# Optimization experiments

Measured on AMD Instinct MI355X. Metric: run time of the kernel, lower is better.

The kernel has to match this reference:

```python
import jax, jax.numpy as jnp
import numpy as np

# ---- dimensions ----
N_MOL, N_PER = 256, 32
N = N_MOL * N_PER                      # 8192 nodes
E = N_MOL * N_PER * (N_PER - 1)        # 253952 fully-connected directed edges
SDIM, VDIM, EDIM = 256, 64, 32
NAF, NBT, LAT = 16, 5, 64
LAYERS = 5
MSG_IN = 2 * SDIM + EDIM + 2           # [s_i, s_j, e, d, a]
MSG_OUT = SDIM + VDIM + 1 + EDIM       # scalar msg, vec weights, pos weight, edge update
BOND_IN = SDIM + EDIM + 1
BOND_HID = 128


def _block_fc_edges():
    # fully-connected (no self loops) edges within each molecule of N_PER atoms
    idx = np.arange(N_PER)
    src, tgt = np.meshgrid(idx, idx, indexing='ij')
    mask = src != tgt
    src, tgt = src[mask], tgt[mask]
    offs = (np.arange(N_MOL) * N_PER)[:, None]
    S = (src[None, :] + offs).reshape(-1)
    T = (tgt[None, :] + offs).reshape(-1)
    return np.stack([S, T], 0).astype(np.int64)


def setup_inputs() -> dict:
    key = jax.random.key(0)
    ks = jax.random.split(key, 16)
    edge_index = jnp.asarray(_block_fc_edges())
    batch = jnp.asarray(np.repeat(np.arange(N_MOL), N_PER).astype(np.int64))
    return dict(
        x=jax.random.normal(ks[0], (N, NAF), jnp.float32),
        z=jax.random.normal(ks[1], (N, LAT), jnp.float32),
        rot=jax.random.normal(ks[2], (N_MOL, 3, 3), jnp.float32),
        edge_index_global=edge_index,
        edge_attr_global=jax.random.normal(ks[3], (E, NBT), jnp.float32),
        batch=batch,
        # atom/bond input mappings (DenseLayer == Linear)
        Wam=jax.random.normal(ks[4], (NAF + LAT, SDIM + 3), jnp.float32) * 0.05,
        bam=jnp.zeros((SDIM + 3,), jnp.float32),
        Wbm=jax.random.normal(ks[5], (NBT, EDIM), jnp.float32) * 0.3,
        bbm=jnp.zeros((EDIM,), jnp.float32),
        # stacked per-layer EQGAT message-MLP weights
        gW1=jax.random.normal(ks[6], (LAYERS, MSG_IN, SDIM), jnp.float32) * 0.03,
        gb1=jnp.zeros((LAYERS, SDIM), jnp.float32),
        gW2=jax.random.normal(ks[7], (LAYERS, SDIM, MSG_OUT), jnp.float32) * 0.05,
        gb2=jnp.zeros((LAYERS, MSG_OUT), jnp.float32),
        # prediction heads
        Wh1=jax.random.normal(ks[8], (SDIM, SDIM), jnp.float32) * 0.05,
        bh1=jnp.zeros((SDIM,), jnp.float32),
        Wh2=jax.random.normal(ks[9], (SDIM, NAF), jnp.float32) * 0.05,
        bh2=jnp.zeros((NAF,), jnp.float32),
        We1=jax.random.normal(ks[10], (BOND_IN, BOND_HID), jnp.float32) * 0.05,
        be1=jnp.zeros((BOND_HID,), jnp.float32),
        We2=jax.random.normal(ks[11], (BOND_HID, NBT), jnp.float32) * 0.05,
        be2=jnp.zeros((NBT,), jnp.float32),
    )


def _edge_attrs(pos, src, tgt):
    # faithful to Decoder.calculate_edge_attrs (sqrt=True)
    r = pos[tgt] - pos[src]                       # [E,3]
    a = jnp.sum(pos[tgt] * pos[src], -1)          # [E]
    d = jnp.sqrt(jnp.clip(jnp.sum(r * r, -1), 1e-6))
    r_norm = r / (1.0 + d)[:, None]
    return d, a, r_norm


def reference(x, z, rot, edge_index_global, edge_attr_global, batch,
              Wam, bam, Wbm, bbm, gW1, gb1, gW2, gb2,
              Wh1, bh1, Wh2, bh2, We1, be1, We2, be2):
    src, tgt = edge_index_global[0], edge_index_global[1]
    n = x.shape[0]
    # atom mapping + split into scalar feats and positions
    h = jnp.concatenate([x, z], -1) @ Wam + bam
    s, pos = h[:, :SDIM], h[:, SDIM:]
    # per-graph rotation of positions
    pos = jnp.einsum('bij,bj->bi', rot[batch], pos)
    # bond mapping
    e = edge_attr_global @ Wbm + bbm
    v = jnp.zeros((n, 3, VDIM), x.dtype)
    # segment-mean denominator (in-degree), fixed since edge_index is fixed
    cnt = jnp.clip(jax.ops.segment_sum(jnp.ones((src.shape[0],), x.dtype), tgt,
                                       num_segments=n), 1.0)

    def seg_mean(m):
        out = jax.ops.segment_sum(m, tgt, num_segments=n)
        return out / cnt.reshape((n,) + (1,) * (m.ndim - 1))

    def layer(carry, p):
        s, v, pos, e = carry
        W1, b1, W2, b2 = p
        d, a, r_norm = _edge_attrs(pos, src, tgt)   # recompute_edge_attributes=True
        feat = jnp.concatenate([s[src], s[tgt], e, d[:, None], a[:, None]], -1)
        hdn = jax.nn.silu(feat @ W1 + b1)
        m = hdn @ W2 + b2
        m_s = m[:, :SDIM]
        m_v = m[:, SDIM:SDIM + VDIM]
        m_p = m[:, SDIM + VDIM:SDIM + VDIM + 1]
        m_e = m[:, SDIM + VDIM + 1:]
        s = s + seg_mean(m_s)                                   # scalar update
        v = v + seg_mean(r_norm[:, :, None] * m_v[:, None, :])  # equivariant vec update
        pos = pos + seg_mean(r_norm * m_p)                      # equivariant pos update
        e = e + m_e                                             # edge feature update
        return (s, v, pos, e), None

    (s, v, pos, e), _ = jax.lax.scan(layer, (s, v, pos, e), (gW1, gb1, gW2, gb2))

    # prediction head: atom logits, bond logits (symmetric s_i+s_j), coords
    atoms = jax.nn.silu(s @ Wh1 + bh1) @ Wh2 + bh2
    d, a, r_norm = _edge_attrs(pos, src, tgt)
    ef = jnp.concatenate([s[src] + s[tgt], e, d[:, None]], -1)
    bonds = jax.nn.silu(ef @ We1 + be1) @ We2 + be2
    return atoms, bonds, pos
```

## Files before the change

### kernel.cpp

```cpp
#include <hip/hip_runtime.h>
#include <hip/hip_bf16.h>
#include <cstdint>
#include <cstddef>

#define N_MOLS 256
#define NN     8192
#define SDIM_  256
#define NAF_   16
#define LAYERS_ 5

typedef __attribute__((ext_vector_type(8)))  short bf16x8;
typedef __attribute__((ext_vector_type(16))) float f32x16;
typedef __attribute__((ext_vector_type(4)))  float f32x4;

__device__ __forceinline__ float silu_f(float x) {
    return x * __builtin_amdgcn_rcpf(1.f + __expf(-x));
}
__device__ __forceinline__ short bfc(float f) {
    __hip_bfloat16 h = __float2bfloat16(f);
    return __builtin_bit_cast(short, h);
}
__device__ __forceinline__ float bf2f(short h) {
    union { uint32_t u; float f; } v; v.u = ((uint32_t)(unsigned short)h) << 16; return v.f;
}
#define ONEBF ((short)0x3F80)

#define OFF_T1    0
#define OFF_W2ST  655360
#define OFF_WH1T  983040
#define OFF_WE1T  1048576
#define OFF_W1CG  1081344
#define OFF_W1DA  1122304
#define OFF_W2P   1124864
#define OFF_W2EI  1126144
#define OFF_WE1CG 1167104
#define OFF_WD    1171200
#define OFF_WE2I  1171328
#define W_TOTAL   1175424

__global__ __launch_bounds__(256) void prep_weights(
    const float* __restrict__ gW1, const float* __restrict__ gW2,
    const float* __restrict__ Wh1, const float* __restrict__ We1,
    const float* __restrict__ We2, short* __restrict__ wb)
{
    for (int o = blockIdx.x * 256 + threadIdx.x; o < W_TOTAL; o += gridDim.x * 256) {
        float v;
        if (o < OFF_W2ST) {
            const int l = o >> 17, r = o & 131071;
            const int j2 = r >> 8, k = r & 255;
            v = gW1[(size_t)l * 139776 + (size_t)((j2 >> 8) * 256 + k) * 256 + (j2 & 255)];
        } else if (o < OFF_WH1T) {
            const int q = o - OFF_W2ST;
            const int l = q >> 16, r = q & 65535;
            const int n = r >> 8, k = r & 255;
            v = gW2[(size_t)l * 90368 + (size_t)k * 353 + n];
        } else if (o < OFF_WE1T) {
            const int q = o - OFF_WH1T;
            v = Wh1[(size_t)(q & 255) * 256 + (q >> 8)];
        } else if (o < OFF_W1CG) {
            const int q = o - OFF_WE1T;
            v = We1[(size_t)(q & 255) * 128 + (q >> 8)];
        } else if (o < OFF_W1DA) {
            const int q = o - OFF_W1CG;
            const int l = q >> 13, r = q & 8191;
            const int j = r >> 5, w = r & 31;
            v = gW1[(size_t)l * 139776 + (size_t)(512 + w) * 256 + j];
        } else if (o < OFF_W2P) {
            const int q = o - OFF_W1DA;
            const int l = q >> 9, r = q & 511;
            v = gW1[(size_t)l * 139776 + (size_t)(544 + (r >> 8)) * 256 + (r & 255)];
        } else if (o < OFF_W2EI) {
            const int q = o - OFF_W2P;
            v = gW2[(size_t)(q >> 8) * 90368 + (size_t)(q & 255) * 353 + 320];
        } else if (o < OFF_WE1CG) {
            const int q = o - OFF_W2EI;
            const int l = q >> 13, r = q & 8191;
            const int kk = r >> 9, lanei = (r >> 3) & 63, jj = r & 7;
            const int j = kk * 16 + (lanei >> 5) * 8 + jj;
            v = gW2[(size_t)l * 90368 + (size_t)j * 353 + 321 + (lanei & 31)];
        } else if (o < OFF_WD) {
            const int q = o - OFF_WE1CG;
            v = We1[(size_t)(256 + (q & 31)) * 128 + (q >> 5)];
        } else if (o < OFF_WE2I) {
            v = We1[288 * 128 + (o - OFF_WD)];
        } else {
            const int q = o - OFF_WE2I;
            const int kk = q >> 9, lanei = (q >> 3) & 63, jj = q & 7;
            const int c = lanei & 31;
            v = (c < 5) ? We2[(size_t)(kk * 16 + (lanei >> 5) * 8 + jj) * 5 + c] : 0.f;
        }
        wb[o] = bfc(v);
    }
}

__global__ __launch_bounds__(256) void node_init2(
    const float* __restrict__ x, const float* __restrict__ z,
    const float* __restrict__ rot, const float* __restrict__ Wam,
    const float* __restrict__ bam, float* __restrict__ s,
    short* __restrict__ sbf, float* __restrict__ pos)
{
    const int mol = blockIdx.x, t = threadIdx.x;
    __shared__ __align__(16) float xz[32][80];
    __shared__ float praw[32][3];
    for (int idx = t; idx < 32 * 80; idx += 256) {
        const int i = idx / 80, k = idx % 80;
        xz[i][k] = (k < 16) ? x[(size_t)(mol * 32 + i) * 16 + k]
                            : z[(size_t)(mol * 32 + i) * 64 + (k - 16)];
    }
    __syncthreads();
    float acc[32];
    #pragma unroll
    for (int i = 0; i < 32; ++i) acc[i] = 0.f;
    for (int k0 = 0; k0 < 80; k0 += 4) {
        const float w0 = Wam[(k0 + 0) * 259 + t];
        const float w1 = Wam[(k0 + 1) * 259 + t];
        const float w2 = Wam[(k0 + 2) * 259 + t];
        const float w3 = Wam[(k0 + 3) * 259 + t];
        #pragma unroll
        for (int i = 0; i < 32; ++i) {
            const float4 xv = *(const float4*)&xz[i][k0];
            acc[i] += xv.x * w0 + xv.y * w1 + xv.z * w2 + xv.w * w3;
        }
    }
    const float bv = bam[t];
    #pragma unroll
    for (int i = 0; i < 32; ++i) {
        const float v = acc[i] + bv;
        s[(size_t)(mol * 32 + i) * 256 + t] = v;
        sbf[(size_t)(mol * 32 + i) * 256 + t] = bfc(v);
    }
    if (t < 96) {
        const int i = t / 3, c = t % 3;
        float a2 = bam[256 + c];
        for (int k = 0; k < 80; ++k) a2 += xz[i][k] * Wam[k * 259 + 256 + c];
        praw[i][c] = a2;
    }
    __syncthreads();
    if (t < 96) {
        const int i = t / 3, c = t % 3;
        float p = 0.f;
        for (int jj = 0; jj < 3; ++jj) p += rot[mol * 9 + c * 3 + jj] * praw[i][jj];
        pos[(size_t)(mol * 32 + i) * 3 + c] = p;
    }
}

__global__ __launch_bounds__(256) void edge_init3(
    const float* __restrict__ ea, const float* __restrict__ Wbm,
    const float* __restrict__ bbm, short* __restrict__ ebuf)
{
    const int mol = blockIdx.x, t = threadIdx.x;
    __shared__ float sEa[4960];
    __shared__ float sW[5][32];
    __shared__ float sB[32];
    const float* base = ea + (size_t)mol * 4960;
    for (int i = t; i < 4960; i += 256) sEa[i] = base[i];
    if (t < 160) sW[t / 32][t & 31] = Wbm[t];
    if (t < 32)  sB[t] = bbm[t];
    __syncthreads();
    for (int i = t; i < 31744; i += 256) {
        const int c = i & 31;
        const int rrn = i >> 5;
        const int n = rrn / 31, rr = rrn - n * 31;
        const int s_ = rr + (rr >= n ? 1 : 0);
        const int gl = s_ * 31 + (n - (n > s_ ? 1 : 0));
        float acc = sB[c];
        #pragma unroll
        for (int k = 0; k < 5; ++k) acc += sEa[gl * 5 + k] * sW[k][c];
        ebuf[(size_t)mol * 31744 + i] = bfc(acc);
    }
}

template<int ACT, int OUTBF>
__global__ __launch_bounds__(256) void gemm_mfma(
    const short* __restrict__ A, const short* __restrict__ BT,
    void* __restrict__ Cv, const float* __restrict__ bias,
    int K, int N, float alpha)
{
    const int n0 = blockIdx.x * 64, m0 = blockIdx.y * 128;
    const int t = threadIdx.x;
    const int wave = t >> 6, lane = t & 63;
    const int l = lane & 31, half = lane >> 5;
    const int wm = wave & 1, wn = wave >> 1;
    __shared__ __align__(16) short sA[128][40];
    __shared__ __align__(16) short sBt[64][40];
    f32x16 acc0 = {}, acc1 = {};
    const int mA = t >> 1, koA = (t & 1) * 16;
    const int nB = t & 63, kqB = (t >> 6) * 8;
    for (int k0 = 0; k0 < K; k0 += 32) {
        {
            const short* ap = A + (size_t)(m0 + mA) * K + k0 + koA;
            *(bf16x8*)&sA[mA][koA]     = *(const bf16x8*)(ap);
            *(bf16x8*)&sA[mA][koA + 8] = *(const bf16x8*)(ap + 8);
        }
        {
            const short* bp = BT + (size_t)(n0 + nB) * K + k0 + kqB;
            *(bf16x8*)&sBt[nB][kqB] = *(const bf16x8*)bp;
        }
        __syncthreads();
        #pragma unroll
        for (int ks = 0; ks < 2; ++ks) {
            const bf16x8 bfrag = *(const bf16x8*)&sBt[wn * 32 + l][ks * 16 + half * 8];
            const bf16x8 afr0  = *(const bf16x8*)&sA[wm * 64 + l][ks * 16 + half * 8];
            const bf16x8 afr1  = *(const bf16x8*)&sA[wm * 64 + 32 + l][ks * 16 + half * 8];
            acc0 = __builtin_amdgcn_mfma_f32_32x32x16_bf16(afr0, bfrag, acc0, 0,0,0);
            acc1 = __builtin_amdgcn_mfma_f32_32x32x16_bf16(afr1, bfrag, acc1, 0,0,0);
        }
        __syncthreads();
    }
    const int n = n0 + wn * 32 + l;
    const float bv = bias ? bias[n] : 0.f;
    #pragma unroll
    for (int r = 0; r < 16; ++r) {
        const int row = (r & 3) + 8 * (r >> 2) + 4 * half;
        #pragma unroll
        for (int h = 0; h < 2; ++h) {
            const int m = m0 + wm * 64 + h * 32 + row;
            float v = alpha * (h ? acc1[r] : acc0[r]) + bv;
            if (ACT) v = silu_f(v);
            if (OUTBF) ((short*)Cv)[(size_t)m * N + n] = bfc(v);
            else       ((float*)Cv)[(size_t)m * N + n] = v;
        }
    }
}

__global__ __launch_bounds__(512) void edge_mfma(
    const short* __restrict__ sbfA, const short* __restrict__ T1,
    const float* __restrict__ posIn, float* __restrict__ posOut,
    short* __restrict__ ebuf,
    const short* __restrict__ W1cG, const short* __restrict__ W1daP,
    const short* __restrict__ W2pP, const short* __restrict__ W2eimg,
    const short* __restrict__ W2sT,
    const float* __restrict__ b1, const float* __restrict__ b2,
    float* __restrict__ s, short* __restrict__ sbfOut)
{
    const int blk = blockIdx.x;
    const int mol = blk >> 1;
    const int nbase = (blk & 1) * 16;
    const int t = threadIdx.x;
    const int wave = t >> 6, lane = t & 63;
    const int l = lane & 31, half = lane >> 5;
    const int node0 = mol * 32;

    __shared__ __align__(16) short sBg[256][72];
    __shared__ __align__(16) short sM[8][32][40];
    __shared__ __align__(16) short sHrows[16][264];
    __shared__ __align__(16) short sSB[16][264];
    __shared__ float sPosS[32][4];
    __shared__ __align__(16) short sW1da[2][256];
    __shared__ __align__(16) short sW2p[256];
    __shared__ float sP[8][32];
    __shared__ float sPd[16][4];
    short* sSbf = &sM[0][0][0];

    {
        const int j = t & 255, gh = t >> 8;
        const bf16x8 v0 = *(const bf16x8*)&W1cG[j * 32 + gh * 16];
        const bf16x8 v1 = *(const bf16x8*)&W1cG[j * 32 + gh * 16 + 8];
        const int c3 = (j >> 3) & 3;
        const int s0 = ((gh * 2 + 0) + 3 * c3) & 7;
        const int s1 = ((gh * 2 + 1) + 3 * c3) & 7;
        *(bf16x8*)&sBg[j][s0 * 8] = v0;
        *(bf16x8*)&sBg[j][s1 * 8] = v1;
    }
    {
        const int row = t >> 4, ch = (t & 15) * 16;
        const short* src = sbfA + (size_t)(node0 + row) * 256 + ch;
        *(bf16x8*)&sSbf[row * 264 + ch]     = *(const bf16x8*)(src);
        *(bf16x8*)&sSbf[row * 264 + ch + 8] = *(const bf16x8*)(src + 8);
    }
    if (t < 64) {
        short* d = &sW1da[0][0];
        *(bf16x8*)&d[t * 8] = *(const bf16x8*)&W1daP[t * 8];
    }
    if (t < 32) *(bf16x8*)&sW2p[t * 8] = *(const bf16x8*)&W2pP[t * 8];
    if (t < 96) sPosS[t / 3][t % 3] = posIn[node0 * 3 + t];
    __syncthreads();

    {
        const int jt = wave;
        const int j = jt * 32 + l;
        f32x16 accA = {}, accB = {};
        #pragma unroll
        for (int k0 = 0; k0 < 256; k0 += 16) {
            const bf16x8 afr = *(const bf16x8*)&sSbf[l * 264 + k0 + half * 8];
            const bf16x8 bA  = *(const bf16x8*)(T1 + (size_t)(j) * 256 + k0 + half * 8);
            const bf16x8 bB  = *(const bf16x8*)(T1 + (size_t)(256 + j) * 256 + k0 + half * 8);
            accA = __builtin_amdgcn_mfma_f32_32x32x16_bf16(afr, bA, accA, 0,0,0);
            accB = __builtin_amdgcn_mfma_f32_32x32x16_bf16(afr, bB, accB, 0,0,0);
        }
        const int c3 = (j >> 3) & 3;
        #pragma unroll
        for (int r = 0; r < 16; ++r) {
            const int node = (r & 3) + 8 * (r >> 2) + 4 * half;
            const int k = 32 + node;
            const int slot = ((k >> 3) + 3 * c3) & 7;
            sBg[j][slot * 8 + (k & 7)] = bfc(accA[r]);
            const int nl = node - nbase;
            if ((unsigned)nl < 16u) sSB[nl][j] = bfc(accB[r]);
        }
    }
    __syncthreads();

    bf16x8 w2efr[16];
    #pragma unroll
    for (int kk = 0; kk < 16; ++kk)
        w2efr[kk] = *(const bf16x8*)&W2eimg[(size_t)(kk * 64 + lane) * 8];
    float b1v[8];
    short w1dv[8], w1av[8];
    #pragma unroll
    for (int cb = 0; cb < 8; ++cb) {
        b1v[cb]  = b1[cb * 32 + l];
        w1dv[cb] = sW1da[0][cb * 32 + l];
        w1av[cb] = sW1da[1][cb * 32 + l];
    }
    const float b2e = b2[321 + l];
    const float b2p = b2[320];
    int bslot[4];
    #pragma unroll
    for (int ks = 0; ks < 4; ++ks)
        bslot[ks] = ((ks * 2 + half) + 3 * ((l >> 3) & 3)) & 7;

    for (int ni = 0; ni < 2; ++ni) {
        const int n = nbase + wave + ni * 8;
        const int nloc = wave + ni * 8;
        const int rrc = (l < 31) ? l : 30;
        const int src = rrc + (rrc >= n ? 1 : 0);
        const float ax = sPosS[n][0],  ay = sPosS[n][1],  az = sPosS[n][2];
        const float bx = sPosS[src][0], by = sPosS[src][1], bz = sPosS[src][2];
        const float rx = ax - bx, ry = ay - by, rz = az - bz;
        const float av = ax * bx + ay * by + az * bz;
        const float dd = sqrtf(fmaxf(rx * rx + ry * ry + rz * rz, 1e-6f));
        const float inv = __builtin_amdgcn_rcpf(1.f + dd);
        const float rnx = rx * inv, rny = ry * inv, rnz = rz * inv;

        const short* ebase = ebuf + ((size_t)((mol * 32 + n) * 31 + l)) * 32;
        const bf16x8 fr0 = *(const bf16x8*)(ebase + half * 8);
        const bf16x8 fr1 = *(const bf16x8*)(ebase + 16 + half * 8);
        bf16x8 fr2 = {}, fr3, fr4;
        if (half == 0) { fr2[0] = bfc(dd); fr2[1] = bfc(av); }
        #pragma unroll
        for (int jj = 0; jj < 8; ++jj) {
            fr3[jj] = (half * 8 + jj == src)      ? ONEBF : (short)0;
            fr4[jj] = (16 + half * 8 + jj == src) ? ONEBF : (short)0;
        }

        f32x16 accC = {}, accP = {};
        float Hacc[8];

        const int g = l >> 3, jlow = l & 7;
        #pragma unroll
        for (int cb = 0; cb < 8; ++cb) {
            const float sbv = bf2f(sSB[nloc][cb * 32 + l]) + b1v[cb];
            f32x16 acc;
            #pragma unroll
            for (int r = 0; r < 16; ++r) acc[r] = sbv;
            {
                const short* brow = &sBg[cb * 32 + l][0];
                __builtin_amdgcn_s_setprio(1);
                acc = __builtin_amdgcn_mfma_f32_32x32x16_bf16(fr0, *(const bf16x8*)(brow + bslot[0]*8), acc, 0,0,0);
                acc = __builtin_amdgcn_mfma_f32_32x32x16_bf16(fr1, *(const bf16x8*)(brow + bslot[1]*8), acc, 0,0,0);
                acc = __builtin_amdgcn_mfma_f32_32x32x16_bf16(fr3, *(const bf16x8*)(brow + bslot[2]*8), acc, 0,0,0);
                acc = __builtin_amdgcn_mfma_f32_32x32x16_bf16(fr4, *(const bf16x8*)(brow + bslot[3]*8), acc, 0,0,0);
                bf16x8 frB2 = {};
                if (half == 0) { frB2[0] = w1dv[cb]; frB2[1] = w1av[cb]; }
                acc = __builtin_amdgcn_mfma_f32_32x32x16_bf16(fr2, frB2, acc, 0,0,0);
                __builtin_amdgcn_s_setprio(0);
            }
            float hs = 0.f;
            #pragma unroll
            for (int r = 0; r < 16; ++r) {
                const int e = (r & 3) + 8 * (r >> 2) + 4 * half;
                float h = silu_f(acc[r]);
                if (half == 1 && r == 15) h = 0.f;
                hs += h;
                sM[wave][e][((g + (e >> 3)) & 3) * 8 + jlow] = bfc(h);
            }
            Hacc[cb] = hs;
            #pragma unroll
            for (int q = 0; q < 2; ++q) {
                const bf16x8 afr  = *(const bf16x8*)&sM[wave][l][((q * 2 + half + (l >> 3)) & 3) * 8];
                const bf16x8 wpfr = *(const bf16x8*)&sW2p[cb * 32 + q * 16 + half * 8];
                accC = __builtin_amdgcn_mfma_f32_32x32x16_bf16(afr, w2efr[cb * 2 + q], accC, 0,0,0);
                accP = __builtin_amdgcn_mfma_f32_32x32x16_bf16(afr, wpfr, accP, 0,0,0);
            }
        }
        #pragma unroll
        for (int cb = 0; cb < 8; ++cb) {
            const float v = Hacc[cb] + __shfl_xor(Hacc[cb], 32, 64);
            if (lane < 32) sHrows[nloc][cb * 32 + lane] = bfc(v);
        }
        if (l == 0) {
            #pragma unroll
            for (int q4 = 0; q4 < 4; ++q4) {
                float4 pv = { accP[q4 * 4 + 0], accP[q4 * 4 + 1],
                              accP[q4 * 4 + 2], accP[q4 * 4 + 3] };
                *(float4*)&sP[wave][q4 * 8 + 4 * half] = pv;
            }
        }
        const float pown = sP[wave][l];
        const float pfull = (half == 0 && l < 31) ? (pown + b2p) : 0.f;
        float pd0 = rnx * pfull, pd1 = rny * pfull, pd2 = rnz * pfull;
        #pragma unroll
        for (int m = 1; m <= 32; m <<= 1) {
            pd0 += __shfl_xor(pd0, m, 64);
            pd1 += __shfl_xor(pd1, m, 64);
            pd2 += __shfl_xor(pd2, m, 64);
        }
        if (lane == 0) {
            sPd[nloc][0] = pd0;
            sPd[nloc][1] = pd1;
            sPd[nloc][2] = pd2;
        }
        #pragma unroll
        for (int r = 0; r < 16; ++r) {
            const int e = (r & 3) + 8 * (r >> 2) + 4 * half;
            if (e < 31) {
                short* ep = ebuf + ((size_t)((mol * 32 + n) * 31 + e)) * 32 + l;
                *ep = bfc(bf2f(*ep) + accC[r] + b2e);
            }
        }
    }

    __syncthreads();

    {
        const int jb0 = wave * 32;
        const int arow = lane & 15, kg = lane >> 4;
        f32x4 accS0 = {}, accS1 = {};
        #pragma unroll
        for (int k0 = 0; k0 < 256; k0 += 32) {
            const bf16x8 afr = *(const bf16x8*)&sHrows[arow][k0 + kg * 8];
            const bf16x8 bf0 = *(const bf16x8*)&W2sT[(size_t)(jb0 + arow) * 256 + k0 + kg * 8];
            const bf16x8 bf1 = *(const bf16x8*)&W2sT[(size_t)(jb0 + 16 + arow) * 256 + k0 + kg * 8];
            accS0 = __builtin_amdgcn_mfma_f32_16x16x32_bf16(afr, bf0, accS0, 0,0,0);
            accS1 = __builtin_amdgcn_mfma_f32_16x16x32_bf16(afr, bf1, accS1, 0,0,0);
        }
        const int col = lane & 15;
        const int orow = (lane >> 4) * 4;
        const float bv0 = b2[jb0 + col];
        const float bv1 = b2[jb0 + 16 + col];
        #pragma unroll
        for (int r = 0; r < 4; ++r) {
            const int node = node0 + nbase + orow + r;
            {
                float* sp = s + (size_t)node * 256 + jb0 + col;
                const float nv = *sp + accS0[r] * (1.f / 31.f) + bv0;
                *sp = nv;
                sbfOut[(size_t)node * 256 + jb0 + col] = bfc(nv);
            }
            {
                float* sp = s + (size_t)node * 256 + jb0 + 16 + col;
                const float nv = *sp + accS1[r] * (1.f / 31.f) + bv1;
                *sp = nv;
                sbfOut[(size_t)node * 256 + jb0 + 16 + col] = bfc(nv);
            }
        }
    }
    if (t < 48) {
        const int nl = t / 3, c = t % 3;
        const int node = node0 + nbase + nl;
        posOut[(size_t)node * 3 + c] = posIn[(size_t)node * 3 + c] + sPd[nl][c] * (1.f / 31.f);
    }
}

__global__ __launch_bounds__(512) void bond_mfma(
    const short* __restrict__ sbfA, const short* __restrict__ We1T,
    const float* __restrict__ pos, short* __restrict__ ebuf,
    const short* __restrict__ We1cG, const short* __restrict__ WdP,
    const short* __restrict__ We2img,
    const float* __restrict__ be1, const float* __restrict__ be2,
    float* __restrict__ outB, float* __restrict__ outPos)
{
    const int blk = blockIdx.x;
    const int mol = blk >> 1;
    const int nbase = (blk & 1) * 16;
    const int t = threadIdx.x;
    const int wave = t >> 6, lane = t & 63;
    const int l = lane & 31, half = lane >> 5;
    const int node0 = mol * 32;

    __shared__ __align__(16) short sBg2[128][72];
    __shared__ __align__(16) short sHdnB[8][32][40];
    __shared__ __align__(16) short sU[32][136];
    __shared__ float sPosS[32][4];
    __shared__ __align__(16) short sWd[128];
    short* sSbf = &sHdnB[0][0][0];

    {
        const int j = t & 127, g = t >> 7;
        const bf16x8 v = *(const bf16x8*)&We1cG[j * 32 + g * 8];
        const int slot = (g + 3 * ((j >> 3) & 3)) & 7;
        *(bf16x8*)&sBg2[j][slot * 8] = v;
    }
    {
        const int row = t >> 4, ch = (t & 15) * 16;
        const short* src = sbfA + (size_t)(node0 + row) * 256 + ch;
        *(bf16x8*)&sSbf[row * 264 + ch]     = *(const bf16x8*)(src);
        *(bf16x8*)&sSbf[row * 264 + ch + 8] = *(const bf16x8*)(src + 8);
    }
    if (t < 16) *(bf16x8*)&sWd[t * 8] = *(const bf16x8*)&WdP[t * 8];
    if (t < 96) sPosS[t / 3][t % 3] = pos[node0 * 3 + t];
    __syncthreads();

    if (wave < 4) {
        const int j = wave * 32 + l;
        f32x16 accU = {};
        #pragma unroll
        for (int k0 = 0; k0 < 256; k0 += 16) {
            const bf16x8 afr = *(const bf16x8*)&sSbf[l * 264 + k0 + half * 8];
            const bf16x8 bU  = *(const bf16x8*)(We1T + (size_t)j * 256 + k0 + half * 8);
            accU = __builtin_amdgcn_mfma_f32_32x32x16_bf16(afr, bU, accU, 0,0,0);
        }
        const int c3 = (j >> 3) & 3;
        #pragma unroll
        for (int r = 0; r < 16; ++r) {
            const int node = (r & 3) + 8 * (r >> 2) + 4 * half;
            const short uv = bfc(accU[r]);
            const int k = 32 + node;
            const int slot = ((k >> 3) + 3 * c3) & 7;
            sBg2[j][slot * 8 + (k & 7)] = uv;
            sU[node][j] = uv;
        }
    }

    bf16x8 w2fr[8];
    #pragma unroll
    for (int kk = 0; kk < 8; ++kk)
        w2fr[kk] = *(const bf16x8*)&We2img[(size_t)(kk * 64 + lane) * 8];
    float be1v[4];
    #pragma unroll
    for (int cb = 0; cb < 4; ++cb) be1v[cb] = be1[cb * 32 + l];
    const float be2v = (l < 5) ? be2[l] : 0.f;
    int bslot[4];
    #pragma unroll
    for (int ks = 0; ks < 4; ++ks)
        bslot[ks] = ((ks * 2 + half) + 3 * ((l >> 3) & 3)) & 7;
    __syncthreads();

    for (int ni = 0; ni < 2; ++ni) {
        const int n = nbase + wave + ni * 8;
        const int rrc = (l < 31) ? l : 30;
        const int src = rrc + (rrc >= n ? 1 : 0);
        const float rx = sPosS[n][0] - sPosS[src][0];
        const float ry = sPosS[n][1] - sPosS[src][1];
        const float rz = sPosS[n][2] - sPosS[src][2];
        const float dd = sqrtf(fmaxf(rx * rx + ry * ry + rz * rz, 1e-6f));

        const short* ebase = ebuf + ((size_t)((mol * 32 + n) * 31 + l)) * 32;
        const bf16x8 fr0 = *(const bf16x8*)(ebase + half * 8);
        const bf16x8 fr1 = *(const bf16x8*)(ebase + 16 + half * 8);
        bf16x8 fr2 = {}, fr3, fr4;
        if (half == 0) fr2[0] = bfc(dd);
        #pragma unroll
        for (int jj = 0; jj < 8; ++jj) {
            fr3[jj] = (half * 8 + jj == src)      ? ONEBF : (short)0;
            fr4[jj] = (16 + half * 8 + jj == src) ? ONEBF : (short)0;
        }

        f32x16 accC = {};
        const int g = l >> 3, jlow = l & 7;
        #pragma unroll
        for (int cb = 0; cb < 4; ++cb) {
            const float uin = bf2f(sU[n][cb * 32 + l]) + be1v[cb];
            f32x16 acc;
            #pragma unroll
            for (int r = 0; r < 16; ++r) acc[r] = uin;
            {
                const short* brow = &sBg2[cb * 32 + l][0];
                acc = __builtin_amdgcn_mfma_f32_32x32x16_bf16(fr0, *(const bf16x8*)(brow + bslot[0]*8), acc, 0,0,0);
                acc = __builtin_amdgcn_mfma_f32_32x32x16_bf16(fr1, *(const bf16x8*)(brow + bslot[1]*8), acc, 0,0,0);
                acc = __builtin_amdgcn_mfma_f32_32x32x16_bf16(fr3, *(const bf16x8*)(brow + bslot[2]*8), acc, 0,0,0);
                acc = __builtin_amdgcn_mfma_f32_32x32x16_bf16(fr4, *(const bf16x8*)(brow + bslot[3]*8), acc, 0,0,0);
                bf16x8 frWd = {};
                if (half == 0) frWd[0] = sWd[cb * 32 + l];
                acc = __builtin_amdgcn_mfma_f32_32x32x16_bf16(fr2, frWd, acc, 0,0,0);
            }
            #pragma unroll
            for (int r = 0; r < 16; ++r) {
                const int e = (r & 3) + 8 * (r >> 2) + 4 * half;
                sHdnB[wave][e][((g + (e >> 3)) & 3) * 8 + jlow] = bfc(silu_f(acc[r]));
            }
            #pragma unroll
            for (int q = 0; q < 2; ++q) {
                const bf16x8 afr = *(const bf16x8*)&sHdnB[wave][l][((q * 2 + half + (l >> 3)) & 3) * 8];
                accC = __builtin_amdgcn_mfma_f32_32x32x16_bf16(afr, w2fr[cb * 2 + q], accC, 0,0,0);
            }
        }
        if (l < 5) {
            #pragma unroll
            for (int r = 0; r < 16; ++r) {
                const int e = (r & 3) + 8 * (r >> 2) + 4 * half;
                if (e < 31) {
                    const int s_ = e + (e >= n ? 1 : 0);
                    const int ge = (mol * 32 + s_) * 31 + (n - (n > s_ ? 1 : 0));
                    outB[(size_t)ge * 5 + l] = accC[r] + be2v;
                }
            }
        }
    }
    if (t < 48) {
        const int nl = t / 3, c = t % 3;
        const int node = node0 + nbase + nl;
        outPos[(size_t)node * 3 + c] = pos[(size_t)node * 3 + c];
    }
}

__global__ __launch_bounds__(256) void atoms_kernel(
    const short* __restrict__ tmp, const float* __restrict__ Wh2,
    const float* __restrict__ bh2, float* __restrict__ outA)
{
    const int t = threadIdx.x;
    __shared__ __align__(16) float sW[256][17];
    for (int i = t; i < 256 * 4; i += 256) {
        const int k = i >> 2, c4 = (i & 3) * 4;
        const float4 w = *(const float4*)&Wh2[k * 16 + c4];
        sW[k][c4 + 0] = w.x; sW[k][c4 + 1] = w.y;
        sW[k][c4 + 2] = w.z; sW[k][c4 + 3] = w.w;
    }
    __syncthreads();
    const int gid = blockIdx.x * 256 + t;
    const int n = gid >> 4, o = gid & 15;
    float acc = bh2[o];
    for (int k0 = 0; k0 < 256; k0 += 8) {
        const bf16x8 a = *(const bf16x8*)&tmp[(size_t)n * 256 + k0];
        #pragma unroll
        for (int j = 0; j < 8; ++j)
            acc += bf2f(a[j]) * sW[k0 + j][o];
    }
    outA[gid] = acc;
}

extern "C" void kernel_launch(void* const* d_in, const int* in_sizes, int n_in,
                              void* d_out, int out_size, void* d_ws, size_t ws_size,
                              hipStream_t stream) {
    const float* x   = (const float*)d_in[0];
    const float* z   = (const float*)d_in[1];
    const float* rot = (const float*)d_in[2];
    const float* ea  = (const float*)d_in[4];
    const float* Wam = (const float*)d_in[6];
    const float* bam = (const float*)d_in[7];
    const float* Wbm = (const float*)d_in[8];
    const float* bbm = (const float*)d_in[9];
    const float* gW1 = (const float*)d_in[10];
    const float* gb1 = (const float*)d_in[11];
    const float* gW2 = (const float*)d_in[12];
    const float* gb2 = (const float*)d_in[13];
    const float* Wh1 = (const float*)d_in[14];
    const float* bh1 = (const float*)d_in[15];
    const float* Wh2 = (const float*)d_in[16];
    const float* bh2 = (const float*)d_in[17];
    const float* We1 = (const float*)d_in[18];
    const float* be1 = (const float*)d_in[19];
    const float* We2 = (const float*)d_in[20];
    const float* be2 = (const float*)d_in[21];
    float* out = (float*)d_out;

    float* ws  = (float*)d_ws;
    float* s    = ws;
    float* pos  = ws + 2097152;
    short* e    = (short*)(ws + 2121728);
    short* wb   = (short*)(ws + 6184960);
    short* sbf0 = (short*)(ws + 6772672);
    short* sbf1 = (short*)(ws + 10248192);
    short* tmph = (short*)(ws + 12345344);
    float* pos2 = ws + 16539648;

    prep_weights<<<1024, 256, 0, stream>>>(gW1, gW2, Wh1, We1, We2, wb);
    node_init2<<<N_MOLS, 256, 0, stream>>>(x, z, rot, Wam, bam, s, sbf0, pos);
    edge_init3<<<N_MOLS, 256, 0, stream>>>(ea, Wbm, bbm, e);

    float* pbuf[2] = { pos, pos2 };
    short* sbb[2] = { sbf0, sbf1 };
    for (int l = 0; l < LAYERS_; ++l) {
        const float* b1 = gb1 + l * 256;
        const float* b2 = gb2 + l * 353;
        edge_mfma<<<2 * N_MOLS, 512, 0, stream>>>(
            sbb[l & 1], wb + OFF_T1 + (size_t)l * 131072,
            pbuf[l & 1], pbuf[(l + 1) & 1], e,
            wb + OFF_W1CG + l * 8192, wb + OFF_W1DA + l * 512,
            wb + OFF_W2P + l * 256, wb + OFF_W2EI + l * 8192,
            wb + OFF_W2ST + (size_t)l * 65536,
            b1, b2, s, sbb[(l + 1) & 1]);
    }
    float* posF = pbuf[LAYERS_ & 1];
    short* sbfF = sbb[LAYERS_ & 1];

    gemm_mfma<1,1><<<dim3(4, 64), 256, 0, stream>>>(
        sbfF, wb + OFF_WH1T, tmph, bh1, 256, 256, 1.f);
    atoms_kernel<<<512, 256, 0, stream>>>(tmph, Wh2, bh2, out);

    bond_mfma<<<2 * N_MOLS, 512, 0, stream>>>(
        sbfF, wb + OFF_WE1T, posF, e, wb + OFF_WE1CG, wb + OFF_WD,
        wb + OFF_WE2I, be1, be2, out + 131072, out + 131072 + 1269760);
}
```

Before: 669.0 us.

## Merge init kernels into one launch and fold atom head into bond kernel

The three setup kernels (weight prep, node init, edge init) become a single launch that picks its role from the block index. The atom prediction head (a 256x256 silu layer followed by a 256x16 layer) moves from a separate GEMM and atoms kernel into the tail of the bond kernel, computed with 16x16 MFMAs on the block's node tile. A bf16 copy of Wh2 is added to the packed weight buffer for this. The aim is to cut kernel launches and the global round trip of the hidden activation, at the cost of a longer bond-kernel epilogue that reuses its shared buffers.

```diff
diff --git a/kernel.cpp b/kernel.cpp
--- a/kernel.cpp
+++ b/kernel.cpp
@@ -36,189 +36,138 @@
 #define OFF_WE1CG 1167104
 #define OFF_WD    1171200
 #define OFF_WE2I  1171328
-#define W_TOTAL   1175424
-
-__global__ __launch_bounds__(256) void prep_weights(
+#define OFF_WH2T  1175424
+#define W_TOTAL   1179520
+
+__global__ __launch_bounds__(256) void init_all(
+    const float* __restrict__ x, const float* __restrict__ z,
+    const float* __restrict__ rot, const float* __restrict__ Wam,
+    const float* __restrict__ bam, const float* __restrict__ ea,
+    const float* __restrict__ Wbm, const float* __restrict__ bbm,
     const float* __restrict__ gW1, const float* __restrict__ gW2,
     const float* __restrict__ Wh1, const float* __restrict__ We1,
-    const float* __restrict__ We2, short* __restrict__ wb)
+    const float* __restrict__ We2, const float* __restrict__ Wh2,
+    float* __restrict__ s, short* __restrict__ sbf, float* __restrict__ pos,
+    short* __restrict__ ebuf, short* __restrict__ wb)
 {
-    for (int o = blockIdx.x * 256 + threadIdx.x; o < W_TOTAL; o += gridDim.x * 256) {
-        float v;
-        if (o < OFF_W2ST) {
-            const int l = o >> 17, r = o & 131071;
-            const int j2 = r >> 8, k = r & 255;
-            v = gW1[(size_t)l * 139776 + (size_t)((j2 >> 8) * 256 + k) * 256 + (j2 & 255)];
-        } else if (o < OFF_WH1T) {
-            const int q = o - OFF_W2ST;
-            const int l = q >> 16, r = q & 65535;
-            const int n = r >> 8, k = r & 255;
-            v = gW2[(size_t)l * 90368 + (size_t)k * 353 + n];
-        } else if (o < OFF_WE1T) {
-            const int q = o - OFF_WH1T;
-            v = Wh1[(size_t)(q & 255) * 256 + (q >> 8)];
-        } else if (o < OFF_W1CG) {
-            const int q = o - OFF_WE1T;
-            v = We1[(size_t)(q & 255) * 128 + (q >> 8)];
-        } else if (o < OFF_W1DA) {
-            const int q = o - OFF_W1CG;
-            const int l = q >> 13, r = q & 8191;
-            const int j = r >> 5, w = r & 31;
-            v = gW1[(size_t)l * 139776 + (size_t)(512 + w) * 256 + j];
-        } else if (o < OFF_W2P) {
-            const int q = o - OFF_W1DA;
-            const int l = q >> 9, r = q & 511;
-            v = gW1[(size_t)l * 139776 + (size_t)(544 + (r >> 8)) * 256 + (r & 255)];
-        } else if (o < OFF_W2EI) {
-            const int q = o - OFF_W2P;
-            v = gW2[(size_t)(q >> 8) * 90368 + (size_t)(q & 255) * 353 + 320];
-        } else if (o < OFF_WE1CG) {
-            const int q = o - OFF_W2EI;
-            const int l = q >> 13, r = q & 8191;
-            const int kk = r >> 9, lanei = (r >> 3) & 63, jj = r & 7;
-            const int j = kk * 16 + (lanei >> 5) * 8 + jj;
-            v = gW2[(size_t)l * 90368 + (size_t)j * 353 + 321 + (lanei & 31)];
-        } else if (o < OFF_WD) {
-            const int q = o - OFF_WE1CG;
-            v = We1[(size_t)(256 + (q & 31)) * 128 + (q >> 5)];
-        } else if (o < OFF_WE2I) {
-            v = We1[288 * 128 + (o - OFF_WD)];
-        } else {
-            const int q = o - OFF_WE2I;
-            const int kk = q >> 9, lanei = (q >> 3) & 63, jj = q & 7;
-            const int c = lanei & 31;
-            v = (c < 5) ? We2[(size_t)(kk * 16 + (lanei >> 5) * 8 + jj) * 5 + c] : 0.f;
-        }
-        wb[o] = bfc(v);
-    }
-}
-
-__global__ __launch_bounds__(256) void node_init2(
-    const float* __restrict__ x, const float* __restrict__ z,
-    const float* __restrict__ rot, const float* __restrict__ Wam,
-    const float* __restrict__ bam, float* __restrict__ s,
-    short* __restrict__ sbf, float* __restrict__ pos)
-{
-    const int mol = blockIdx.x, t = threadIdx.x;
-    __shared__ __align__(16) float xz[32][80];
-    __shared__ float praw[32][3];
-    for (int idx = t; idx < 32 * 80; idx += 256) {
-        const int i = idx / 80, k = idx % 80;
-        xz[i][k] = (k < 16) ? x[(size_t)(mol * 32 + i) * 16 + k]
-                            : z[(size_t)(mol * 32 + i) * 64 + (k - 16)];
-    }
-    __syncthreads();
-    float acc[32];
-    #pragma unroll
-    for (int i = 0; i < 32; ++i) acc[i] = 0.f;
-    for (int k0 = 0; k0 < 80; k0 += 4) {
-        const float w0 = Wam[(k0 + 0) * 259 + t];
-        const float w1 = Wam[(k0 + 1) * 259 + t];
-        const float w2 = Wam[(k0 + 2) * 259 + t];
-        const float w3 = Wam[(k0 + 3) * 259 + t];
+    __shared__ __align__(16) char smem[20608];
+    const int b = blockIdx.x, t = threadIdx.x;
+    if (b < 1024) {
+        for (int o = b * 256 + t; o < W_TOTAL; o += 1024 * 256) {
+            float v;
+            if (o < OFF_W2ST) {
+                const int l = o >> 17, r = o & 131071;
+                const int j2 = r >> 8, k = r & 255;
+                v = gW1[(size_t)l * 139776 + (size_t)((j2 >> 8) * 256 + k) * 256 + (j2 & 255)];
+            } else if (o < OFF_WH1T) {
+                const int q = o - OFF_W2ST;
+                const int l = q >> 16, r = q & 65535;
+                const int n = r >> 8, k = r & 255;
+                v = gW2[(size_t)l * 90368 + (size_t)k * 353 + n];
+            } else if (o < OFF_WE1T) {
+                const int q = o - OFF_WH1T;
+                v = Wh1[(size_t)(q & 255) * 256 + (q >> 8)];
+            } else if (o < OFF_W1CG) {
+                const int q = o - OFF_WE1T;
+                v = We1[(size_t)(q & 255) * 128 + (q >> 8)];
+            } else if (o < OFF_W1DA) {
+                const int q = o - OFF_W1CG;
+                const int l = q >> 13, r = q & 8191;
+                const int j = r >> 5, w = r & 31;
+                v = gW1[(size_t)l * 139776 + (size_t)(512 + w) * 256 + j];
+            } else if (o < OFF_W2P) {
+                const int q = o - OFF_W1DA;
+                const int l = q >> 9, r = q & 511;
+                v = gW1[(size_t)l * 139776 + (size_t)(544 + (r >> 8)) * 256 + (r & 255)];
+            } else if (o < OFF_W2EI) {
+                const int q = o - OFF_W2P;
+                v = gW2[(size_t)(q >> 8) * 90368 + (size_t)(q & 255) * 353 + 320];
+            } else if (o < OFF_WE1CG) {
+                const int q = o - OFF_W2EI;
+                const int l = q >> 13, r = q & 8191;
+                const int kk = r >> 9, lanei = (r >> 3) & 63, jj = r & 7;
+                const int j = kk * 16 + (lanei >> 5) * 8 + jj;
+                v = gW2[(size_t)l * 90368 + (size_t)j * 353 + 321 + (lanei & 31)];
+            } else if (o < OFF_WD) {
+                const int q = o - OFF_WE1CG;
+                v = We1[(size_t)(256 + (q & 31)) * 128 + (q >> 5)];
+            } else if (o < OFF_WE2I) {
+                v = We1[288 * 128 + (o - OFF_WD)];
+            } else if (o < OFF_WH2T) {
+                const int q = o - OFF_WE2I;
+                const int kk = q >> 9, lanei = (q >> 3) & 63, jj = q & 7;
+                const int c = lanei & 31;
+                v = (c < 5) ? We2[(size_t)(kk * 16 + (lanei >> 5) * 8 + jj) * 5 + c] : 0.f;
+            } else {
+                const int q = o - OFF_WH2T;
+                v = Wh2[(size_t)(q & 255) * 16 + (q >> 8)];
+            }
+            wb[o] = bfc(v);
+        }
+    } else if (b < 1280) {
+        const int mol = b - 1024;
+        float (*xz)[80]  = (float(*)[80])smem;
+        float (*praw)[3] = (float(*)[3])(smem + 32 * 80 * 4);
+        for (int idx = t; idx < 32 * 80; idx += 256) {
+            const int i = idx / 80, k = idx % 80;
+            xz[i][k] = (k < 16) ? x[(size_t)(mol * 32 + i) * 16 + k]
+                                : z[(size_t)(mol * 32 + i) * 64 + (k - 16)];
+        }
+        __syncthreads();
+        float acc[32];
+        #pragma unroll
+        for (int i = 0; i < 32; ++i) acc[i] = 0.f;
+        for (int k0 = 0; k0 < 80; k0 += 4) {
+            const float w0 = Wam[(k0 + 0) * 259 + t];
+            const float w1 = Wam[(k0 + 1) * 259 + t];
+            const float w2 = Wam[(k0 + 2) * 259 + t];
+            const float w3 = Wam[(k0 + 3) * 259 + t];
+            #pragma unroll
+            for (int i = 0; i < 32; ++i) {
+                const float4 xv = *(const float4*)&xz[i][k0];
+                acc[i] += xv.x * w0 + xv.y * w1 + xv.z * w2 + xv.w * w3;
+            }
+        }
+        const float bv = bam[t];
         #pragma unroll
         for (int i = 0; i < 32; ++i) {
-            const float4 xv = *(const float4*)&xz[i][k0];
-            acc[i] += xv.x * w0 + xv.y * w1 + xv.z * w2 + xv.w * w3;
-        }
-    }
-    const float bv = bam[t];
-    #pragma unroll
-    for (int i = 0; i < 32; ++i) {
-        const float v = acc[i] + bv;
-        s[(size_t)(mol * 32 + i) * 256 + t] = v;
-        sbf[(size_t)(mol * 32 + i) * 256 + t] = bfc(v);
-    }
-    if (t < 96) {
-        const int i = t / 3, c = t % 3;
-        float a2 = bam[256 + c];
-        for (int k = 0; k < 80; ++k) a2 += xz[i][k] * Wam[k * 259 + 256 + c];
-        praw[i][c] = a2;
-    }
-    __syncthreads();
-    if (t < 96) {
-        const int i = t / 3, c = t % 3;
-        float p = 0.f;
-        for (int jj = 0; jj < 3; ++jj) p += rot[mol * 9 + c * 3 + jj] * praw[i][jj];
-        pos[(size_t)(mol * 32 + i) * 3 + c] = p;
-    }
-}
-
-__global__ __launch_bounds__(256) void edge_init3(
-    const float* __restrict__ ea, const float* __restrict__ Wbm,
-    const float* __restrict__ bbm, short* __restrict__ ebuf)
-{
-    const int mol = blockIdx.x, t = threadIdx.x;
-    __shared__ float sEa[4960];
-    __shared__ float sW[5][32];
-    __shared__ float sB[32];
-    const float* base = ea + (size_t)mol * 4960;
-    for (int i = t; i < 4960; i += 256) sEa[i] = base[i];
-    if (t < 160) sW[t / 32][t & 31] = Wbm[t];
-    if (t < 32)  sB[t] = bbm[t];
-    __syncthreads();
-    for (int i = t; i < 31744; i += 256) {
-        const int c = i & 31;
-        const int rrn = i >> 5;
-        const int n = rrn / 31, rr = rrn - n * 31;
-        const int s_ = rr + (rr >= n ? 1 : 0);
-        const int gl = s_ * 31 + (n - (n > s_ ? 1 : 0));
-        float acc = sB[c];
-        #pragma unroll
-        for (int k = 0; k < 5; ++k) acc += sEa[gl * 5 + k] * sW[k][c];
-        ebuf[(size_t)mol * 31744 + i] = bfc(acc);
-    }
-}
-
-template<int ACT, int OUTBF>
-__global__ __launch_bounds__(256) void gemm_mfma(
-    const short* __restrict__ A, const short* __restrict__ BT,
-    void* __restrict__ Cv, const float* __restrict__ bias,
-    int K, int N, float alpha)
-{
-    const int n0 = blockIdx.x * 64, m0 = blockIdx.y * 128;
-    const int t = threadIdx.x;
-    const int wave = t >> 6, lane = t & 63;
-    const int l = lane & 31, half = lane >> 5;
-    const int wm = wave & 1, wn = wave >> 1;
-    __shared__ __align__(16) short sA[128][40];
-    __shared__ __align__(16) short sBt[64][40];
-    f32x16 acc0 = {}, acc1 = {};
-    const int mA = t >> 1, koA = (t & 1) * 16;
-    const int nB = t & 63, kqB = (t >> 6) * 8;
-    for (int k0 = 0; k0 < K; k0 += 32) {
-        {
-            const short* ap = A + (size_t)(m0 + mA) * K + k0 + koA;
-            *(bf16x8*)&sA[mA][koA]     = *(const bf16x8*)(ap);
-            *(bf16x8*)&sA[mA][koA + 8] = *(const bf16x8*)(ap + 8);
-        }
-        {
-            const short* bp = BT + (size_t)(n0 + nB) * K + k0 + kqB;
-            *(bf16x8*)&sBt[nB][kqB] = *(const bf16x8*)bp;
+            const float v = acc[i] + bv;
+            s[(size_t)(mol * 32 + i) * 256 + t] = v;
+            sbf[(size_t)(mol * 32 + i) * 256 + t] = bfc(v);
+        }
+        if (t < 96) {
+            const int i = t / 3, c = t % 3;
+            float a2 = bam[256 + c];
+            for (int k = 0; k < 80; ++k) a2 += xz[i][k] * Wam[k * 259 + 256 + c];
+            praw[i][c] = a2;
         }
         __syncthreads();
-        #pragma unroll
-        for (int ks = 0; ks < 2; ++ks) {
-            const bf16x8 bfrag = *(const bf16x8*)&sBt[wn * 32 + l][ks * 16 + half * 8];
-            const bf16x8 afr0  = *(const bf16x8*)&sA[wm * 64 + l][ks * 16 + half * 8];
-            const bf16x8 afr1  = *(const bf16x8*)&sA[wm * 64 + 32 + l][ks * 16 + half * 8];
-            acc0 = __builtin_amdgcn_mfma_f32_32x32x16_bf16(afr0, bfrag, acc0, 0,0,0);
-            acc1 = __builtin_amdgcn_mfma_f32_32x32x16_bf16(afr1, bfrag, acc1, 0,0,0);
-        }
+        if (t < 96) {
+            const int i = t / 3, c = t % 3;
+            float p = 0.f;
+            for (int jj = 0; jj < 3; ++jj) p += rot[mol * 9 + c * 3 + jj] * praw[i][jj];
+            pos[(size_t)(mol * 32 + i) * 3 + c] = p;
+        }
+    } else {
+        const int mol = b - 1280;
+        float* sEa      = (float*)smem;
+        float (*sW)[32] = (float(*)[32])(smem + 4960 * 4);
+        float* sB       = (float*)(smem + (4960 + 160) * 4);
+        const float* base = ea + (size_t)mol * 4960;
+        for (int i = t; i < 4960; i += 256) sEa[i] = base[i];
+        if (t < 160) sW[t / 32][t & 31] = Wbm[t];
+        if (t < 32)  sB[t] = bbm[t];
         __syncthreads();
-    }
-    const int n = n0 + wn * 32 + l;
-    const float bv = bias ? bias[n] : 0.f;
-    #pragma unroll
-    for (int r = 0; r < 16; ++r) {
-        const int row = (r & 3) + 8 * (r >> 2) + 4 * half;
-        #pragma unroll
-        for (int h = 0; h < 2; ++h) {
-            const int m = m0 + wm * 64 + h * 32 + row;
-            float v = alpha * (h ? acc1[r] : acc0[r]) + bv;
-            if (ACT) v = silu_f(v);
-            if (OUTBF) ((short*)Cv)[(size_t)m * N + n] = bfc(v);
-            else       ((float*)Cv)[(size_t)m * N + n] = v;
+        for (int i = t; i < 31744; i += 256) {
+            const int c = i & 31;
+            const int rrn = i >> 5;
+            const int n = rrn / 31, rr = rrn - n * 31;
+            const int s_ = rr + (rr >= n ? 1 : 0);
+            const int gl = s_ * 31 + (n - (n > s_ ? 1 : 0));
+            float acc = sB[c];
+            #pragma unroll
+            for (int k = 0; k < 5; ++k) acc += sEa[gl * 5 + k] * sW[k][c];
+            ebuf[(size_t)mol * 31744 + i] = bfc(acc);
         }
     }
 }
@@ -467,9 +416,12 @@
     const short* __restrict__ sbfA, const short* __restrict__ We1T,
     const float* __restrict__ pos, short* __restrict__ ebuf,
     const short* __restrict__ We1cG, const short* __restrict__ WdP,
-    const short* __restrict__ We2img,
+    const short* __restrict__ We2img, const short* __restrict__ Wh1T,
+    const short* __restrict__ Wh2I,
     const float* __restrict__ be1, const float* __restrict__ be2,
-    float* __restrict__ outB, float* __restrict__ outPos)
+    const float* __restrict__ bh1, const float* __restrict__ bh2,
+    float* __restrict__ outA, float* __restrict__ outB,
+    float* __restrict__ outPos)
 {
     const int blk = blockIdx.x;
     const int mol = blk >> 1;
@@ -603,31 +555,54 @@
         const int node = node0 + nbase + nl;
         outPos[(size_t)node * 3 + c] = pos[(size_t)node * 3 + c];
     }
-}
-
-__global__ __launch_bounds__(256) void atoms_kernel(
-    const short* __restrict__ tmp, const float* __restrict__ Wh2,
-    const float* __restrict__ bh2, float* __restrict__ outA)
-{
-    const int t = threadIdx.x;
-    __shared__ __align__(16) float sW[256][17];
-    for (int i = t; i < 256 * 4; i += 256) {
-        const int k = i >> 2, c4 = (i & 3) * 4;
-        const float4 w = *(const float4*)&Wh2[k * 16 + c4];
-        sW[k][c4 + 0] = w.x; sW[k][c4 + 1] = w.y;
-        sW[k][c4 + 2] = w.z; sW[k][c4 + 3] = w.w;
-    }
-    __syncthreads();
-    const int gid = blockIdx.x * 256 + t;
-    const int n = gid >> 4, o = gid & 15;
-    float acc = bh2[o];
-    for (int k0 = 0; k0 < 256; k0 += 8) {
-        const bf16x8 a = *(const bf16x8*)&tmp[(size_t)n * 256 + k0];
-        #pragma unroll
-        for (int j = 0; j < 8; ++j)
-            acc += bf2f(a[j]) * sW[k0 + j][o];
-    }
-    outA[gid] = acc;
+
+    __syncthreads();
+    {
+        short* sA3 = &sU[0][0];
+        const int row = t >> 5, ch = (t & 31) * 8;
+        *(bf16x8*)&sA3[row * 264 + ch] =
+            *(const bf16x8*)(sbfA + (size_t)(node0 + nbase + row) * 256 + ch);
+    }
+    __syncthreads();
+    {
+        short* sA3 = &sU[0][0];
+        short* sT  = &sBg2[0][0];
+        const int jb0 = wave * 32;
+        const int arow = lane & 15, kg = lane >> 4;
+        f32x4 a0 = {}, a1 = {};
+        #pragma unroll
+        for (int k0 = 0; k0 < 256; k0 += 32) {
+            const bf16x8 afr = *(const bf16x8*)&sA3[arow * 264 + k0 + kg * 8];
+            const bf16x8 bw0 = *(const bf16x8*)(Wh1T + (size_t)(jb0 + arow) * 256 + k0 + kg * 8);
+            const bf16x8 bw1 = *(const bf16x8*)(Wh1T + (size_t)(jb0 + 16 + arow) * 256 + k0 + kg * 8);
+            a0 = __builtin_amdgcn_mfma_f32_16x16x32_bf16(afr, bw0, a0, 0,0,0);
+            a1 = __builtin_amdgcn_mfma_f32_16x16x32_bf16(afr, bw1, a1, 0,0,0);
+        }
+        const int col = lane & 15, orow = (lane >> 4) * 4;
+        const float bva = bh1[jb0 + col], bvb = bh1[jb0 + 16 + col];
+        #pragma unroll
+        for (int r = 0; r < 4; ++r) {
+            sT[(orow + r) * 264 + jb0 + col]      = bfc(silu_f(a0[r] + bva));
+            sT[(orow + r) * 264 + jb0 + 16 + col] = bfc(silu_f(a1[r] + bvb));
+        }
+    }
+    __syncthreads();
+    if (wave == 0) {
+        short* sT = &sBg2[0][0];
+        const int arow = lane & 15, kg = lane >> 4;
+        f32x4 a2 = {};
+        #pragma unroll
+        for (int k0 = 0; k0 < 256; k0 += 32) {
+            const bf16x8 afr = *(const bf16x8*)&sT[arow * 264 + k0 + kg * 8];
+            const bf16x8 bfr = *(const bf16x8*)(Wh2I + (size_t)arow * 256 + k0 + kg * 8);
+            a2 = __builtin_amdgcn_mfma_f32_16x16x32_bf16(afr, bfr, a2, 0,0,0);
+        }
+        const int col = lane & 15, orow = (lane >> 4) * 4;
+        const float bv = bh2[col];
+        #pragma unroll
+        for (int r = 0; r < 4; ++r)
+            outA[(size_t)(node0 + nbase + orow + r) * 16 + col] = a2[r] + bv;
+    }
 }
 
 extern "C" void kernel_launch(void* const* d_in, const int* in_sizes, int n_in,
@@ -660,14 +635,12 @@
     float* pos  = ws + 2097152;
     short* e    = (short*)(ws + 2121728);
     short* wb   = (short*)(ws + 6184960);
-    short* sbf0 = (short*)(ws + 6772672);
+    short* sbf0 = (short*)(ws + 6774784);
     short* sbf1 = (short*)(ws + 10248192);
-    short* tmph = (short*)(ws + 12345344);
     float* pos2 = ws + 16539648;
 
-    prep_weights<<<1024, 256, 0, stream>>>(gW1, gW2, Wh1, We1, We2, wb);
-    node_init2<<<N_MOLS, 256, 0, stream>>>(x, z, rot, Wam, bam, s, sbf0, pos);
-    edge_init3<<<N_MOLS, 256, 0, stream>>>(ea, Wbm, bbm, e);
+    init_all<<<1536, 256, 0, stream>>>(x, z, rot, Wam, bam, ea, Wbm, bbm,
+        gW1, gW2, Wh1, We1, We2, Wh2, s, sbf0, pos, e, wb);
 
     float* pbuf[2] = { pos, pos2 };
     short* sbb[2] = { sbf0, sbf1 };
@@ -685,11 +658,8 @@
     float* posF = pbuf[LAYERS_ & 1];
     short* sbfF = sbb[LAYERS_ & 1];
 
-    gemm_mfma<1,1><<<dim3(4, 64), 256, 0, stream>>>(
-        sbfF, wb + OFF_WH1T, tmph, bh1, 256, 256, 1.f);
-    atoms_kernel<<<512, 256, 0, stream>>>(tmph, Wh2, bh2, out);
-
     bond_mfma<<<2 * N_MOLS, 512, 0, stream>>>(
         sbfF, wb + OFF_WE1T, posF, e, wb + OFF_WE1CG, wb + OFF_WD,
-        wb + OFF_WE2I, be1, be2, out + 131072, out + 131072 + 1269760);
+        wb + OFF_WE2I, wb + OFF_WH1T, wb + OFF_WH2T,
+        be1, be2, bh1, bh2, out, out + 131072, out + 131072 + 1269760);
 }
```

Measured after the change: 649.9 us. 2.9% less time.
